# Kernel tuning notes

Measured on AMD Instinct MI355X. Metric: run time of the kernel, lower is better.

## Reference

```python
import jax, jax.numpy as jnp
import numpy as np

BS, CIN, COUT, OUT_DIM, S, S0 = 64, 128, 128, 1024, 2, 1
BLK = S * (S0 + 1)  # 4
D = OUT_DIM * BLK   # 4096


def setup_inputs() -> dict:
    key = jax.random.key(0)
    kx, kw = jax.random.split(key)
    x = jax.random.normal(kx, (BS, CIN, D), dtype=jnp.float32)
    weight = jax.random.normal(kw, (COUT, CIN, D), dtype=jnp.float32)
    return {"x": x, "weight": weight}


def reference(x, weight):
    # Equivalent to: (x[:, None] * weight).reshape(bs, cout, cin, out_dim, blk).sum((-1, -3)) / sqrt(cin)
    bs, cin, d = x.shape
    cout = weight.shape[0]
    blk = BLK
    xr = x.reshape(bs, cin, d // blk, blk)          # (bs, cin, out_dim, blk)
    wr = weight.reshape(cout, cin, d // blk, blk)   # (cout, cin, out_dim, blk)
    # Blocked locally-connected contraction over (cin, blk), fused -- never
    # materializes the (bs, cout, cin, d) broadcast intermediate.
    out = jnp.einsum('bink,oink->bon', xr, wr)
    return out / jnp.sqrt(jnp.asarray(cin, dtype=x.dtype))
```

## Files before the change

kernel.cpp:

```cpp
#include <hip/hip_runtime.h>


#define CIN    128
#define COUT   128
#define ODIM   1024
#define DDIM   4096
#define NB     8
#define CI     8
#define NCH    16
#define RS     256

typedef short  bf16x8 __attribute__((ext_vector_type(8)));
typedef short  s16x4  __attribute__((ext_vector_type(4)));
typedef float  f32x4  __attribute__((ext_vector_type(4)));

static __device__ __forceinline__ unsigned short f2bf(float f) {
    unsigned int u = __float_as_uint(f);
    u += 0x7fffu + ((u >> 16) & 1u);
    return (unsigned short)(u >> 16);
}
static __device__ __forceinline__ s16x4 cvt4(float4 v) {
    s16x4 s;
    s[0] = (short)f2bf(v.x); s[1] = (short)f2bf(v.y);
    s[2] = (short)f2bf(v.z); s[3] = (short)f2bf(v.w);
    return s;
}

__global__ __launch_bounds__(1024, 4)
void nolc_kernel(const float* __restrict__ xg,
                 const float* __restrict__ wg,
                 float* __restrict__ outg) {
    __shared__ short xs[2][64 * RS];
    __shared__ short ws[2][64 * RS];

    const int bid  = blockIdx.x;
    const int gidx = (bid & 7) * 32 + (bid >> 3);
    const int bng  = gidx >> 1;
    const int oh   = gidx & 1;

    const int t    = threadIdx.x;
    const int lane = t & 63;
    const int wave = t >> 6;
    const int bq   = wave & 3;
    const int oq   = wave >> 2;
    const int row  = lane & 15;
    const int kg   = lane >> 4;

    const int dbase = 32 * bng;

    const int sn4  = t & 7;
    const int sii  = (t >> 3) & 7;
    const int srow = t >> 6;
    const size_t ITS  = (size_t)16 * CIN * DDIM;
    const size_t CSTR = (size_t)CI * DDIM;

    const float* xp = xg + (size_t)(srow * CIN + sii) * DDIM + dbase + 4 * sn4;
    const float* wp = wg + ((size_t)(oh * 64 + srow) * CIN + sii) * DDIM + dbase + 4 * sn4;

    const int spiece = sn4 * 4 + (sii >> 1);
    const int ldso = srow * RS + (((spiece ^ (srow & 7))) << 3) + (sii & 1) * 4;

    f32x4 acc[NB];
#pragma unroll
    for (int n = 0; n < NB; ++n) acc[n] = (f32x4){0.f, 0.f, 0.f, 0.f};

    float4 rxA[4], rwA[4], rxB[4], rwB[4];

#define LOADC(rx, rw, c)                                                      \
    do {                                                                      \
        const float* _xp = xp + (size_t)(c) * CSTR;                           \
        const float* _wp = wp + (size_t)(c) * CSTR;                           \
        _Pragma("unroll")                                                     \
        for (int it = 0; it < 4; ++it) {                                      \
            rx[it] = *reinterpret_cast<const float4*>(_xp + it * ITS);        \
            rw[it] = *reinterpret_cast<const float4*>(_wp + it * ITS);        \
        }                                                                     \
    } while (0)

#define STAGE(rx, rw, sel)                                                    \
    do {                                                                      \
        _Pragma("unroll")                                                     \
        for (int it = 0; it < 4; ++it) {                                      \
            *reinterpret_cast<s16x4*>(&xs[sel][ldso + it * 16 * RS]) = cvt4(rx[it]); \
            *reinterpret_cast<s16x4*>(&ws[sel][ldso + it * 16 * RS]) = cvt4(rw[it]); \
        }                                                                     \
    } while (0)

    const int xrb = (bq * 16 + row) * RS;
    const int wrb = (oq * 16 + row) * RS;
    const int r8  = row & 7;

#define COMPUTE(sel)                                                          \
    do {                                                                      \
        _Pragma("unroll")                                                     \
        for (int n = 0; n < NB; ++n) {                                        \
            const int po = ((n * 4 + kg) ^ r8) * 8;                           \
            bf16x8 a  = *reinterpret_cast<const bf16x8*>(&xs[sel][xrb + po]); \
            bf16x8 bb = *reinterpret_cast<const bf16x8*>(&ws[sel][wrb + po]); \
            acc[n] = __builtin_amdgcn_mfma_f32_16x16x32_bf16(a, bb, acc[n], 0, 0, 0); \
        }                                                                     \
    } while (0)

    LOADC(rxA, rwA, 0);
    for (int c = 0; c < NCH; c += 2) {
        LOADC(rxB, rwB, c + 1);
        STAGE(rxA, rwA, 0);
        asm volatile("s_waitcnt lgkmcnt(0)" ::: "memory");
        __builtin_amdgcn_s_barrier();
        COMPUTE(0);

        if (c + 2 < NCH) LOADC(rxA, rwA, c + 2);
        STAGE(rxB, rwB, 1);
        asm volatile("s_waitcnt lgkmcnt(0)" ::: "memory");
        __builtin_amdgcn_s_barrier();
        COMPUTE(1);
    }
#undef LOADC
#undef STAGE
#undef COMPUTE

    const float scale = 0.08838834764831845f;
    const int o = oh * 64 + oq * 16 + row;
    const int n0 = 8 * bng;
#pragma unroll
    for (int r = 0; r < 4; ++r) {
        const int b = bq * 16 + kg * 4 + r;
        float* op = outg + ((size_t)b * COUT + o) * ODIM + n0;
        float4 v0, v1;
        v0.x = acc[0][r] * scale; v0.y = acc[1][r] * scale;
        v0.z = acc[2][r] * scale; v0.w = acc[3][r] * scale;
        v1.x = acc[4][r] * scale; v1.y = acc[5][r] * scale;
        v1.z = acc[6][r] * scale; v1.w = acc[7][r] * scale;
        *reinterpret_cast<float4*>(op)     = v0;
        *reinterpret_cast<float4*>(op + 4) = v1;
    }
}

extern "C" void kernel_launch(void* const* d_in, const int* in_sizes, int n_in,
                              void* d_out, int out_size, void* d_ws, size_t ws_size,
                              hipStream_t stream) {
    const float* x = (const float*)d_in[0];
    const float* w = (const float*)d_in[1];
    float* out = (float*)d_out;
    nolc_kernel<<<dim3(256), dim3(1024), 0, stream>>>(x, w, out);
}
```

Baseline: 132.8 us.

## Retile to 512 blocks of 512 threads with single LDS buffer and wider n-tile

Changes the work decomposition from 256 blocks of 1024 threads, each covering all 64 batches and 64 output channels over 8 output positions, to 512 blocks of 512 threads, each covering 32 batches and 32 output channels over 16 positions. Shared memory becomes one buffer with a new XOR swizzle. The loop now stages x and w in separate phases with a trailing barrier instead of ping-ponging two buffers. The aim is finer-grained parallelism and more blocks per CU at the same total bytes loaded. The cost is that x and w are each re-read by more blocks (4x for x, 2x for w), and dropping the double buffer adds an extra barrier per chunk.

```diff
diff --git a/kernel.cpp b/kernel.cpp
--- a/kernel.cpp
+++ b/kernel.cpp
@@ -1,18 +1,18 @@
 #include <hip/hip_runtime.h>
 
 
-#define CIN    128
-#define COUT   128
-#define ODIM   1024
-#define DDIM   4096
-#define NB     8
-#define CI     8
-#define NCH    16
-#define RS     256
+#define CIN  128
+#define COUT 128
+#define ODIM 1024
+#define DDIM 4096
+#define NB   16
+#define CI   8
+#define NCH  16
+#define RS   512
 
-typedef short  bf16x8 __attribute__((ext_vector_type(8)));
-typedef short  s16x4  __attribute__((ext_vector_type(4)));
-typedef float  f32x4  __attribute__((ext_vector_type(4)));
+typedef short bf16x8 __attribute__((ext_vector_type(8)));
+typedef short s16x4  __attribute__((ext_vector_type(4)));
+typedef float f32x4  __attribute__((ext_vector_type(4)));
 
 static __device__ __forceinline__ unsigned short f2bf(float f) {
     unsigned int u = __float_as_uint(f);
@@ -26,106 +26,113 @@
     return s;
 }
 
-__global__ __launch_bounds__(1024, 4)
+__global__ __launch_bounds__(512, 4)
 void nolc_kernel(const float* __restrict__ xg,
                  const float* __restrict__ wg,
                  float* __restrict__ outg) {
-    __shared__ short xs[2][64 * RS];
-    __shared__ short ws[2][64 * RS];
+    __shared__ short lds[64 * RS];
 
     const int bid  = blockIdx.x;
-    const int gidx = (bid & 7) * 32 + (bid >> 3);
-    const int bng  = gidx >> 1;
-    const int oh   = gidx & 1;
+    const int gidx = (bid & 7) * 64 + (bid >> 3);
+    const int ng   = gidx >> 3;
+    const int bq   = (gidx >> 2) & 1;
+    const int oq   = gidx & 3;
 
     const int t    = threadIdx.x;
     const int lane = t & 63;
     const int wave = t >> 6;
-    const int bq   = wave & 3;
-    const int oq   = wave >> 2;
-    const int row  = lane & 15;
-    const int kg   = lane >> 4;
 
-    const int dbase = 32 * bng;
+    const int sn = t & 15;
+    const int si = (t >> 4) & 7;
+    const int rl = t >> 7;
+    const size_t R4 = (size_t)4 * CIN * DDIM;
+    const size_t CH = (size_t)CI * DDIM;
 
-    const int sn4  = t & 7;
-    const int sii  = (t >> 3) & 7;
-    const int srow = t >> 6;
-    const size_t ITS  = (size_t)16 * CIN * DDIM;
-    const size_t CSTR = (size_t)CI * DDIM;
+    const float* px = xg + ((size_t)(bq * 32 + rl) * CIN + si) * DDIM + ng * 64 + sn * 4;
+    const float* pw = wg + ((size_t)(oq * 32 + rl) * CIN + si) * DDIM + ng * 64 + sn * 4;
 
-    const float* xp = xg + (size_t)(srow * CIN + sii) * DDIM + dbase + 4 * sn4;
-    const float* wp = wg + ((size_t)(oh * 64 + srow) * CIN + sii) * DDIM + dbase + 4 * sn4;
+    const int bt  = wave & 1;
+    const int ot  = (wave >> 1) & 1;
+    const int nh  = wave >> 2;
+    const int r16 = lane & 15;
+    const int kg  = lane >> 4;
 
-    const int spiece = sn4 * 4 + (sii >> 1);
-    const int ldso = srow * RS + (((spiece ^ (srow & 7))) << 3) + (sii & 1) * 4;
+    f32x4 acc[8];
+#pragma unroll
+    for (int n = 0; n < 8; ++n) acc[n] = (f32x4){0.f, 0.f, 0.f, 0.f};
 
-    f32x4 acc[NB];
-#pragma unroll
-    for (int n = 0; n < NB; ++n) acc[n] = (f32x4){0.f, 0.f, 0.f, 0.f};
+    float4 rx[8], rw[8];
 
-    float4 rxA[4], rwA[4], rxB[4], rwB[4];
+#define LOADX(c)                                                              \
+    do {                                                                      \
+        const float* _p = px + (size_t)(c) * CH;                              \
+        _Pragma("unroll")                                                     \
+        for (int it = 0; it < 8; ++it)                                        \
+            rx[it] = *reinterpret_cast<const float4*>(_p + it * R4);          \
+    } while (0)
 
-#define LOADC(rx, rw, c)                                                      \
+#define LOADW(c)                                                              \
     do {                                                                      \
-        const float* _xp = xp + (size_t)(c) * CSTR;                           \
-        const float* _wp = wp + (size_t)(c) * CSTR;                           \
+        const float* _p = pw + (size_t)(c) * CH;                              \
         _Pragma("unroll")                                                     \
-        for (int it = 0; it < 4; ++it) {                                      \
-            rx[it] = *reinterpret_cast<const float4*>(_xp + it * ITS);        \
-            rw[it] = *reinterpret_cast<const float4*>(_wp + it * ITS);        \
+        for (int it = 0; it < 8; ++it)                                        \
+            rw[it] = *reinterpret_cast<const float4*>(_p + it * R4);          \
+    } while (0)
+
+#define STAGEX()                                                              \
+    do {                                                                      \
+        _Pragma("unroll")                                                     \
+        for (int it = 0; it < 8; ++it) {                                      \
+            const int row = it * 4 + rl;                                      \
+            *reinterpret_cast<s16x4*>(                                        \
+                &lds[row * RS + si * 64 + ((sn ^ (row & 15)) << 2)]) = cvt4(rx[it]); \
         }                                                                     \
     } while (0)
 
-#define STAGE(rx, rw, sel)                                                    \
+#define STAGEW()                                                              \
     do {                                                                      \
         _Pragma("unroll")                                                     \
-        for (int it = 0; it < 4; ++it) {                                      \
-            *reinterpret_cast<s16x4*>(&xs[sel][ldso + it * 16 * RS]) = cvt4(rx[it]); \
-            *reinterpret_cast<s16x4*>(&ws[sel][ldso + it * 16 * RS]) = cvt4(rw[it]); \
+        for (int it = 0; it < 8; ++it) {                                      \
+            const int row = 32 + it * 4 + rl;                                 \
+            *reinterpret_cast<s16x4*>(                                        \
+                &lds[row * RS + si * 64 + ((sn ^ (row & 15)) << 2)]) = cvt4(rw[it]); \
         }                                                                     \
     } while (0)
 
-    const int xrb = (bq * 16 + row) * RS;
-    const int wrb = (oq * 16 + row) * RS;
-    const int r8  = row & 7;
+    const int xbase = (bt * 16 + r16) * RS;
+    const int wbase = (32 + ot * 16 + r16) * RS;
 
-#define COMPUTE(sel)                                                          \
-    do {                                                                      \
-        _Pragma("unroll")                                                     \
-        for (int n = 0; n < NB; ++n) {                                        \
-            const int po = ((n * 4 + kg) ^ r8) * 8;                           \
-            bf16x8 a  = *reinterpret_cast<const bf16x8*>(&xs[sel][xrb + po]); \
-            bf16x8 bb = *reinterpret_cast<const bf16x8*>(&ws[sel][wrb + po]); \
-            acc[n] = __builtin_amdgcn_mfma_f32_16x16x32_bf16(a, bb, acc[n], 0, 0, 0); \
-        }                                                                     \
-    } while (0)
-
-    LOADC(rxA, rwA, 0);
-    for (int c = 0; c < NCH; c += 2) {
-        LOADC(rxB, rwB, c + 1);
-        STAGE(rxA, rwA, 0);
+    LOADX(0);
+#pragma unroll 1
+    for (int c = 0; c < NCH; ++c) {
+        LOADW(c);
+        STAGEX();
+        if (c + 1 < NCH) LOADX(c + 1);
+        STAGEW();
         asm volatile("s_waitcnt lgkmcnt(0)" ::: "memory");
         __builtin_amdgcn_s_barrier();
-        COMPUTE(0);
 
-        if (c + 2 < NCH) LOADC(rxA, rwA, c + 2);
-        STAGE(rxB, rwB, 1);
-        asm volatile("s_waitcnt lgkmcnt(0)" ::: "memory");
-        __builtin_amdgcn_s_barrier();
-        COMPUTE(1);
+#pragma unroll
+        for (int nn = 0; nn < 8; ++nn) {
+            const int n  = nh * 8 + nn;
+            const int so = (n ^ r16) << 2;
+            s16x4 a0 = *reinterpret_cast<const s16x4*>(&lds[xbase + (kg * 2) * 64 + so]);
+            s16x4 a1 = *reinterpret_cast<const s16x4*>(&lds[xbase + (kg * 2 + 1) * 64 + so]);
+            s16x4 b0 = *reinterpret_cast<const s16x4*>(&lds[wbase + (kg * 2) * 64 + so]);
+            s16x4 b1 = *reinterpret_cast<const s16x4*>(&lds[wbase + (kg * 2 + 1) * 64 + so]);
+            bf16x8 A = __builtin_shufflevector(a0, a1, 0, 1, 2, 3, 4, 5, 6, 7);
+            bf16x8 B = __builtin_shufflevector(b0, b1, 0, 1, 2, 3, 4, 5, 6, 7);
+            acc[nn] = __builtin_amdgcn_mfma_f32_16x16x32_bf16(A, B, acc[nn], 0, 0, 0);
+        }
+        if (c + 1 < NCH) __builtin_amdgcn_s_barrier();
     }
-#undef LOADC
-#undef STAGE
-#undef COMPUTE
 
     const float scale = 0.08838834764831845f;
-    const int o = oh * 64 + oq * 16 + row;
-    const int n0 = 8 * bng;
+    const int o = oq * 32 + ot * 16 + r16;
 #pragma unroll
     for (int r = 0; r < 4; ++r) {
-        const int b = bq * 16 + kg * 4 + r;
-        float* op = outg + ((size_t)b * COUT + o) * ODIM + n0;
+        const int b = bq * 32 + bt * 16 + kg * 4 + r;
+        float* op = outg + ((size_t)b * COUT + o) * ODIM + ng * 16 + nh * 8;
         float4 v0, v1;
         v0.x = acc[0][r] * scale; v0.y = acc[1][r] * scale;
         v0.z = acc[2][r] * scale; v0.w = acc[3][r] * scale;
@@ -134,6 +141,10 @@
         *reinterpret_cast<float4*>(op)     = v0;
         *reinterpret_cast<float4*>(op + 4) = v1;
     }
+#undef LOADX
+#undef LOADW
+#undef STAGEX
+#undef STAGEW
 }
 
 extern "C" void kernel_launch(void* const* d_in, const int* in_sizes, int n_in,
@@ -142,5 +153,5 @@
     const float* x = (const float*)d_in[0];
     const float* w = (const float*)d_in[1];
     float* out = (float*)d_out;
-    nolc_kernel<<<dim3(256), dim3(1024), 0, stream>>>(x, w, out);
+    nolc_kernel<<<dim3(512), dim3(512), 0, stream>>>(x, w, out);
 }
```

Result: slower. 140.5 us (+5.8%).
